# Kernel tuning notes

Measured on AMD Instinct MI355X. Metric: run time of the kernel, lower is better.

Reference implementation:

```python
import jax, jax.numpy as jnp
import numpy as np

DIM = 768
NUM_HEADS = 12
HEAD_DIM = DIM // NUM_HEADS
SCALE = HEAD_DIM ** -0.5
N, B = 1024, 8


def setup_inputs() -> dict:
    key = jax.random.key(0)
    ks = jax.random.split(key, 10)
    s = 0.02
    return {
        "q": jax.random.normal(ks[0], (N, B, DIM), jnp.float32),
        "k": jax.random.normal(ks[1], (N, B, DIM), jnp.float32),
        "v": jax.random.normal(ks[2], (N, B, DIM), jnp.float32),
        "v_img": jax.random.normal(ks[3], (N, B, DIM), jnp.float32),
        "Wq": jax.random.normal(ks[4], (DIM, DIM), jnp.float32) * s,
        "Wk": jax.random.normal(ks[5], (DIM, DIM), jnp.float32) * s,
        "Wv": jax.random.normal(ks[6], (DIM, DIM), jnp.float32) * s,
        "Wvim": jax.random.normal(ks[7], (DIM, DIM), jnp.float32) * s,
        "Wp": jax.random.normal(ks[8], (DIM, DIM), jnp.float32) * s,
        "bp": jnp.zeros((DIM,), jnp.float32),
        "Wpi": jax.random.normal(ks[9], (DIM, DIM), jnp.float32) * s,
        "bpi": jnp.zeros((DIM,), jnp.float32),
    }


def _heads(x):
    # [B, N, C] -> [B, H, N, Dh]
    b, n, _ = x.shape
    return x.reshape(b, n, NUM_HEADS, HEAD_DIM).transpose(0, 2, 1, 3)


def _merge(x):
    # [B, H, N, Dh] -> [B, N, C]
    b, h, n, d = x.shape
    return x.transpose(0, 2, 1, 3).reshape(b, n, h * d)


def reference(q, k, v, v_img, Wq, Wk, Wv, Wvim, Wp, bp, Wpi, bpi):
    # seq-first [N, B, C] -> batch-first [B, N, C]
    qb = jnp.transpose(q, (1, 0, 2)) @ Wq.T
    kb = jnp.transpose(k, (1, 0, 2)) @ Wk.T
    vb = jnp.transpose(v, (1, 0, 2)) @ Wv.T
    vib = jnp.transpose(v_img, (1, 0, 2)) @ Wvim.T

    qh, kh, vh, vih = _heads(qb), _heads(kb), _heads(vb), _heads(vib)

    # shared attention matrix, reused for both value streams
    attn = jnp.einsum("bhqd,bhkd->bhqk", qh, kh) * SCALE
    attn = jax.nn.softmax(attn, axis=-1)

    x = _merge(jnp.einsum("bhqk,bhkd->bhqd", attn, vh)) @ Wp.T + bp
    x_im = _merge(jnp.einsum("bhqk,bhkd->bhqd", attn, vih)) @ Wpi.T + bpi
    return (x, x_im)
```

## Files before the change

kernel.cpp:

```cpp
#include <hip/hip_runtime.h>

#define NSEQ 1024
#define BATCH 8
#define DIMC 768
#define NH 12
#define HD 64
#define SEG 6291456
#define WSEG 589824

typedef __attribute__((ext_vector_type(4))) float f32x4;
typedef __attribute__((ext_vector_type(8))) short s16x8;
typedef __attribute__((ext_vector_type(8))) __bf16 bf16x8;

#define GLL16(gsrc, ldst) __builtin_amdgcn_global_load_lds( \
    (const __attribute__((address_space(1))) unsigned int*)(const void*)(gsrc), \
    (__attribute__((address_space(3))) unsigned int*)(void*)(ldst), 16, 0, 0)

__device__ __forceinline__ short f2bf(float f) {
  union { float f; unsigned u; } v; v.f = f;
  unsigned r = (v.u + 0x7FFFu + ((v.u >> 16) & 1u)) >> 16;
  return (short)r;
}

__device__ __forceinline__ short f2bf1(float f) {
  unsigned r;
  asm("v_cvt_pk_bf16_f32 %0, %1, %2" : "=v"(r) : "v"(f), "v"(0.f));
  return (short)r;
}

__device__ __forceinline__ f32x4 mfma16(bf16x8 a, bf16x8 b, f32x4 c) {
  return __builtin_amdgcn_mfma_f32_16x16x32_bf16(a, b, c, 0, 0, 0);
}

__global__ __launch_bounds__(256) void k_cvt4(
    const float* __restrict__ a0, const float* __restrict__ a1,
    const float* __restrict__ a2, const float* __restrict__ a3,
    short* __restrict__ b0, short* __restrict__ b1,
    short* __restrict__ b2, short* __restrict__ b3, int n4) {
  const float* src; short* dst;
  switch (blockIdx.y) {
    case 0: src = a0; dst = b0; break;
    case 1: src = a1; dst = b1; break;
    case 2: src = a2; dst = b2; break;
    default: src = a3; dst = b3; break;
  }
  int i = blockIdx.x * 256 + threadIdx.x;
  if (i >= n4) return;
  float4 f = reinterpret_cast<const float4*>(src)[i];
  short4 o;
  o.x = f2bf(f.x); o.y = f2bf(f.y); o.z = f2bf(f.z); o.w = f2bf(f.w);
  reinterpret_cast<short4*>(dst)[i] = o;
}

__global__ __launch_bounds__(256) void k_proj(
    const short* __restrict__ x0, const short* __restrict__ x1,
    const short* __restrict__ x2, const short* __restrict__ x3,
    const short* __restrict__ w0, const short* __restrict__ w1,
    const short* __restrict__ w2, const short* __restrict__ w3,
    short* __restrict__ y0, short* __restrict__ y1,
    short* __restrict__ y2, short* __restrict__ y3) {
  __shared__ __align__(16) short SM[32768];
  const int tid = threadIdx.x;
  const int lane = tid & 63;
  const int w = tid >> 6;
  const int wm = w >> 1, wn = w & 1;
  const int nt = blockIdx.x, mt = blockIdx.y, s = blockIdx.z;
  const short *X, *W; short* Y;
  if (s == 0)      { X = x0; W = w0; Y = y0; }
  else if (s == 1) { X = x1; W = w1; Y = y1; }
  else if (s == 2) { X = x2; W = w2; Y = y2; }
  else             { X = x3; W = w3; Y = y3; }

  f32x4 acc[4][4];
#pragma unroll
  for (int mi = 0; mi < 4; ++mi)
#pragma unroll
    for (int ni = 0; ni < 4; ++ni) acc[mi][ni] = (f32x4){0.f, 0.f, 0.f, 0.f};

#define PROJ_STAGE(BUF, KT) do { \
  _Pragma("unroll") for (int ii = 0; ii < 4; ++ii) { \
    int g = ii * 256 + tid; \
    int o = g * 16; \
    int r = o >> 7; \
    int c0 = ((o & 127) ^ ((r & 7) << 4)) >> 1; \
    int m = mt * 128 + r; \
    GLL16(X + ((size_t)((m & 1023) * BATCH + (m >> 10))) * DIMC + (KT) * 64 + c0, \
          (char*)(SM + (BUF) * 8192) + o); \
    GLL16(W + (size_t)(nt * 128 + r) * DIMC + (KT) * 64 + c0, \
          (char*)(SM + 16384 + (BUF) * 8192) + o); \
  } \
} while (0)

  PROJ_STAGE(0, 0);
  __syncthreads();
  int buf = 0;
  for (int kt = 0; kt < 12; ++kt) {
    if (kt < 11) PROJ_STAGE(buf ^ 1, kt + 1);
    const char* As = (const char*)(SM + buf * 8192);
    const char* Bs = (const char*)(SM + 16384 + buf * 8192);
#pragma unroll
    for (int kk = 0; kk < 2; ++kk) {
      bf16x8 a[4], b[4];
      int ce = kk * 32 + (lane >> 4) * 8;
#pragma unroll
      for (int mi = 0; mi < 4; ++mi) {
        int ra = wm * 64 + mi * 16 + (lane & 15);
        int byte = ((ra << 7) + (ce << 1)) ^ ((ra & 7) << 4);
        a[mi] = *(const bf16x8*)(As + byte);
      }
#pragma unroll
      for (int ni = 0; ni < 4; ++ni) {
        int rb = wn * 64 + ni * 16 + (lane & 15);
        int byte = ((rb << 7) + (ce << 1)) ^ ((rb & 7) << 4);
        b[ni] = *(const bf16x8*)(Bs + byte);
      }
#pragma unroll
      for (int mi = 0; mi < 4; ++mi)
#pragma unroll
        for (int ni = 0; ni < 4; ++ni)
          acc[mi][ni] = mfma16(a[mi], b[ni], acc[mi][ni]);
    }
    __syncthreads();
    buf ^= 1;
  }
#undef PROJ_STAGE

  if (s < 2) {
#pragma unroll
    for (int mi = 0; mi < 4; ++mi)
#pragma unroll
      for (int ni = 0; ni < 4; ++ni)
#pragma unroll
        for (int j = 0; j < 4; ++j) {
          int m = mt * 128 + wm * 64 + mi * 16 + (lane >> 4) * 4 + j;
          int dc = nt * 128 + wn * 64 + ni * 16 + (lane & 15);
          int b_ = m >> 10, n_ = m & 1023;
          int h_ = dc >> 6, d_ = dc & 63;
          Y[((size_t)(b_ * NH + h_) * NSEQ + n_) * HD + d_] = f2bf(acc[mi][ni][j]);
        }
  } else {
    __syncthreads();
    short* Ts = SM;
#pragma unroll
    for (int mi = 0; mi < 4; ++mi)
#pragma unroll
      for (int ni = 0; ni < 4; ++ni)
#pragma unroll
        for (int j = 0; j < 4; ++j) {
          int lm = wm * 64 + mi * 16 + (lane >> 4) * 4 + j;
          int ldc = wn * 64 + ni * 16 + (lane & 15);
          int swc = ldc ^ (lm & 126);
          Ts[lm * 128 + swc] = f2bf(acc[mi][ni][j]);
        }
    __syncthreads();
    int l2 = lane * 2;
#pragma unroll 4
    for (int it = 0; it < 32; ++it) {
      int ldc = it * 4 + w;
      short2 pk;
      pk.x = Ts[l2 * 128 + (ldc ^ (l2 & 126))];
      pk.y = Ts[(l2 + 1) * 128 + (ldc ^ ((l2 + 1) & 126))];
      int dc = nt * 128 + ldc;
      int h_ = dc >> 6, d_ = dc & 63;
      int m = mt * 128 + l2;
      int b_ = m >> 10, n_ = m & 1023;
      *(short2*)(Y + ((size_t)(b_ * NH + h_) * HD + d_) * NSEQ + n_) = pk;
    }
  }
}

__global__ __launch_bounds__(256) void k_attn(
    const short* __restrict__ qh, const short* __restrict__ kh,
    const short* __restrict__ vt, const short* __restrict__ vit,
    short* __restrict__ xo, short* __restrict__ xio) {
  __shared__ __align__(16) short Ks[2][4096];
  __shared__ __align__(16) short Vs[2][4096];
  __shared__ __align__(16) short Vis[2][4096];
  __shared__ __align__(16) short Pl[4][2048];

  const int tid = threadIdx.x;
  const int lane = tid & 63;
  const int w = tid >> 6;
  const int blk = blockIdx.x;
  const int virt = (blk & 7) * 96 + (blk >> 3);
  const int bh = virt >> 3;
  const int qt = virt & 7;
  const float CF = 0.125f * 1.44269504f;

  const short* qbase = qh + ((size_t)bh * NSEQ + qt * 128 + w * 32) * HD;
  bf16x8 qf[2][2];
#pragma unroll
  for (int mi = 0; mi < 2; ++mi)
#pragma unroll
    for (int kq = 0; kq < 2; ++kq)
      qf[mi][kq] = *(const bf16x8*)(qbase + (mi * 16 + (lane & 15)) * HD + kq * 32 + (lane >> 4) * 8);

  bf16x8 onesf;
#pragma unroll
  for (int i = 0; i < 8; ++i) onesf[i] = (__bf16)1.0f;

  f32x4 o_[2][4], oi_[2][4], l_acc[2];
#pragma unroll
  for (int mi = 0; mi < 2; ++mi) {
    l_acc[mi] = (f32x4){0.f, 0.f, 0.f, 0.f};
#pragma unroll
    for (int x = 0; x < 4; ++x) {
      o_[mi][x] = (f32x4){0.f, 0.f, 0.f, 0.f};
      oi_[mi][x] = (f32x4){0.f, 0.f, 0.f, 0.f};
    }
  }

  const short* khb = kh + (size_t)bh * NSEQ * HD;
  const short* vtb = vt + (size_t)bh * NSEQ * HD;
  const short* vitb = vit + (size_t)bh * NSEQ * HD;
  char* PlW = (char*)&Pl[w][0];

#define ATTN_STAGE(BUF, KT) do { \
  _Pragma("unroll") for (int ii = 0; ii < 2; ++ii) { \
    int g = ii * 256 + tid; \
    int o = g * 16; \
    int r = o >> 7; \
    int c0 = ((o & 127) ^ ((r & 7) << 4)) >> 1; \
    GLL16(khb + (size_t)((KT) * 64 + r) * HD + c0, (char*)&Ks[BUF][0] + o); \
    GLL16(vtb + (size_t)r * NSEQ + (KT) * 64 + c0, (char*)&Vs[BUF][0] + o); \
    GLL16(vitb + (size_t)r * NSEQ + (KT) * 64 + c0, (char*)&Vis[BUF][0] + o); \
  } \
} while (0)

  ATTN_STAGE(0, 0);
  __syncthreads();
  int buf = 0;
  for (int kt = 0; kt < 16; ++kt) {
    if (kt < 15) ATTN_STAGE(buf ^ 1, kt + 1);
    const char* KsB = (const char*)&Ks[buf][0];
    const char* VsB = (const char*)&Vs[buf][0];
    const char* VisB = (const char*)&Vis[buf][0];

#pragma unroll
    for (int ni = 0; ni < 4; ++ni) {
      f32x4 s0 = (f32x4){0.f, 0.f, 0.f, 0.f};
      f32x4 s1 = (f32x4){0.f, 0.f, 0.f, 0.f};
#pragma unroll
      for (int kk = 0; kk < 2; ++kk) {
        int ce = kk * 32 + (lane >> 4) * 8;
        int rb = ni * 16 + (lane & 15);
        int byte = ((rb << 7) + (ce << 1)) ^ ((rb & 7) << 4);
        bf16x8 kfr = *(const bf16x8*)(KsB + byte);
        s0 = mfma16(qf[0][kk], kfr, s0);
        s1 = mfma16(qf[1][kk], kfr, s1);
      }
#pragma unroll
      for (int j = 0; j < 4; ++j) {
        float p0 = exp2f(s0[j] * CF);
        float p1 = exp2f(s1[j] * CF);
        int rw0 = (lane >> 4) * 4 + j;
        int col = ni * 16 + (lane & 15);
        int b0 = ((rw0 << 7) + (col << 1)) ^ ((rw0 & 7) << 4);
        int b1 = (((rw0 + 16) << 7) + (col << 1)) ^ ((rw0 & 7) << 4);
        *(short*)(PlW + b0) = f2bf1(p0);
        *(short*)(PlW + b1) = f2bf1(p1);
      }
    }

#pragma unroll
    for (int kk = 0; kk < 2; ++kk) {
      int co = kk * 32 + (lane >> 4) * 8;
      int r0 = lane & 15;
      int bp0 = ((r0 << 7) + (co << 1)) ^ ((r0 & 7) << 4);
      int bp1 = (((r0 + 16) << 7) + (co << 1)) ^ ((r0 & 7) << 4);
      bf16x8 pa0 = *(const bf16x8*)(PlW + bp0);
      bf16x8 pa1 = *(const bf16x8*)(PlW + bp1);
      l_acc[0] = mfma16(pa0, onesf, l_acc[0]);
      l_acc[1] = mfma16(pa1, onesf, l_acc[1]);
#pragma unroll
      for (int nd = 0; nd < 4; ++nd) {
        int rv = nd * 16 + (lane & 15);
        int byte = ((rv << 7) + (co << 1)) ^ ((rv & 7) << 4);
        bf16x8 vb = *(const bf16x8*)(VsB + byte);
        bf16x8 vib = *(const bf16x8*)(VisB + byte);
        o_[0][nd] = mfma16(pa0, vb, o_[0][nd]);
        o_[1][nd] = mfma16(pa1, vb, o_[1][nd]);
        oi_[0][nd] = mfma16(pa0, vib, oi_[0][nd]);
        oi_[1][nd] = mfma16(pa1, vib, oi_[1][nd]);
      }
    }
    __syncthreads();
    buf ^= 1;
  }
#undef ATTN_STAGE

#pragma unroll
  for (int mi = 0; mi < 2; ++mi)
#pragma unroll
    for (int j = 0; j < 4; ++j) {
      float inv = 1.0f / l_acc[mi][j];
      int n_ = qt * 128 + w * 32 + mi * 16 + (lane >> 4) * 4 + j;
      size_t base = ((size_t)bh * NSEQ + n_) * HD;
#pragma unroll
      for (int nd = 0; nd < 4; ++nd) {
        int d_ = nd * 16 + (lane & 15);
        xo[base + d_] = f2bf1(o_[mi][nd][j] * inv);
        xio[base + d_] = f2bf1(oi_[mi][nd][j] * inv);
      }
    }
}

__global__ __launch_bounds__(256) void k_outproj(
    const short* __restrict__ xa, const short* __restrict__ xb,
    const short* __restrict__ wa, const short* __restrict__ wb,
    const float* __restrict__ ba, const float* __restrict__ bb,
    float* __restrict__ out) {
  __shared__ __align__(16) short SM[32768];
  const int tid = threadIdx.x;
  const int lane = tid & 63;
  const int w = tid >> 6;
  const int wm = w >> 1, wn = w & 1;
  const int nt = blockIdx.x, mt = blockIdx.y, s = blockIdx.z;
  const short* X = (s == 0) ? xa : xb;
  const short* W = (s == 0) ? wa : wb;
  const float* bias = (s == 0) ? ba : bb;
  float* O = out + (size_t)s * SEG;

  f32x4 acc[4][4];
#pragma unroll
  for (int mi = 0; mi < 4; ++mi)
#pragma unroll
    for (int ni = 0; ni < 4; ++ni) acc[mi][ni] = (f32x4){0.f, 0.f, 0.f, 0.f};

#define OUTP_STAGE(BUF, KT) do { \
  _Pragma("unroll") for (int ii = 0; ii < 4; ++ii) { \
    int g = ii * 256 + tid; \
    int o = g * 16; \
    int r = o >> 7; \
    int c0 = ((o & 127) ^ ((r & 7) << 4)) >> 1; \
    int m = mt * 128 + r; \
    GLL16(X + (((size_t)(m >> 10) * NH + (KT)) * NSEQ + (m & 1023)) * HD + c0, \
          (char*)(SM + (BUF) * 8192) + o); \
    GLL16(W + (size_t)(nt * 128 + r) * DIMC + (KT) * 64 + c0, \
          (char*)(SM + 16384 + (BUF) * 8192) + o); \
  } \
} while (0)

  OUTP_STAGE(0, 0);
  __syncthreads();
  int buf = 0;
  for (int kt = 0; kt < 12; ++kt) {
    if (kt < 11) OUTP_STAGE(buf ^ 1, kt + 1);
    const char* As = (const char*)(SM + buf * 8192);
    const char* Bs = (const char*)(SM + 16384 + buf * 8192);
#pragma unroll
    for (int kk = 0; kk < 2; ++kk) {
      bf16x8 a[4], b[4];
      int ce = kk * 32 + (lane >> 4) * 8;
#pragma unroll
      for (int mi = 0; mi < 4; ++mi) {
        int ra = wm * 64 + mi * 16 + (lane & 15);
        int byte = ((ra << 7) + (ce << 1)) ^ ((ra & 7) << 4);
        a[mi] = *(const bf16x8*)(As + byte);
      }
#pragma unroll
      for (int ni = 0; ni < 4; ++ni) {
        int rb = wn * 64 + ni * 16 + (lane & 15);
        int byte = ((rb << 7) + (ce << 1)) ^ ((rb & 7) << 4);
        b[ni] = *(const bf16x8*)(Bs + byte);
      }
#pragma unroll
      for (int mi = 0; mi < 4; ++mi)
#pragma unroll
        for (int ni = 0; ni < 4; ++ni)
          acc[mi][ni] = mfma16(a[mi], b[ni], acc[mi][ni]);
    }
    __syncthreads();
    buf ^= 1;
  }
#undef OUTP_STAGE

#pragma unroll
  for (int mi = 0; mi < 4; ++mi)
#pragma unroll
    for (int ni = 0; ni < 4; ++ni)
#pragma unroll
      for (int j = 0; j < 4; ++j) {
        int m = mt * 128 + wm * 64 + mi * 16 + (lane >> 4) * 4 + j;
        int dc = nt * 128 + wn * 64 + ni * 16 + (lane & 15);
        O[(size_t)m * DIMC + dc] = acc[mi][ni][j] + bias[dc];
      }
}

extern "C" void kernel_launch(void* const* d_in, const int* in_sizes, int n_in,
                              void* d_out, int out_size, void* d_ws, size_t ws_size,
                              hipStream_t stream) {
  (void)in_sizes; (void)n_in; (void)out_size; (void)ws_size;
  const float* q    = (const float*)d_in[0];
  const float* k    = (const float*)d_in[1];
  const float* v    = (const float*)d_in[2];
  const float* vimg = (const float*)d_in[3];
  const float* Wq   = (const float*)d_in[4];
  const float* Wk   = (const float*)d_in[5];
  const float* Wv   = (const float*)d_in[6];
  const float* Wvim = (const float*)d_in[7];
  const float* Wp   = (const float*)d_in[8];
  const float* bp   = (const float*)d_in[9];
  const float* Wpi  = (const float*)d_in[10];
  const float* bpi  = (const float*)d_in[11];

  short* ws = (short*)d_ws;
  short* xq  = ws;
  short* xk  = ws + (size_t)SEG;
  short* xv  = ws + (size_t)2 * SEG;
  short* xvi = ws + (size_t)3 * SEG;
  short* wqb  = ws + (size_t)4 * SEG;
  short* wkb  = wqb + WSEG;
  short* wvb  = wkb + WSEG;
  short* wvib = wvb + WSEG;
  short* wpb  = wvib + WSEG;
  short* wpib = wpb + WSEG;
  short* qh  = ws + (size_t)4 * SEG + 6 * (size_t)WSEG;
  short* kh  = qh + (size_t)SEG;
  short* vht = kh + (size_t)SEG;
  short* viht = vht + (size_t)SEG;
  short* xo  = viht + (size_t)SEG;
  short* xio = xo + (size_t)SEG;

  k_cvt4<<<dim3(SEG / 4 / 256, 4), 256, 0, stream>>>(q, k, v, vimg, xq, xk, xv, xvi, SEG / 4);
  k_cvt4<<<dim3(WSEG / 4 / 256, 4), 256, 0, stream>>>(Wq, Wk, Wv, Wvim, wqb, wkb, wvb, wvib, WSEG / 4);
  k_cvt4<<<dim3(WSEG / 4 / 256, 2), 256, 0, stream>>>(Wp, Wpi, Wp, Wpi, wpb, wpib, wpb, wpib, WSEG / 4);

  k_proj<<<dim3(6, 64, 4), 256, 0, stream>>>(xq, xk, xv, xvi, wqb, wkb, wvb, wvib, qh, kh, vht, viht);

  k_attn<<<dim3(768), 256, 0, stream>>>(qh, kh, vht, viht, xo, xio);

  k_outproj<<<dim3(6, 64, 2), 256, 0, stream>>>(xo, xio, wpb, wpib, bp, bpi, (float*)d_out);
}
```

Before: 340.3 us.

## Keep softmax probabilities in registers via permlane swaps and fold scale into Wq

The attention kernel no longer writes exponentiated scores to LDS and reads them back. It swaps the QK^T MFMA operand order so results come out transposed, packs pairs to bf16 with v_cvt_pk_bf16_f32, and rearranges them with v_permlane32/16_swap to form PV operands directly in registers. The softmax scale times log2(e) is folded into the Wq bf16 conversion, which removes a multiply per score but changes where rounding happens. The projection grids are also reordered so blockIdx.x walks M tiles, which changes L2 reuse of weights versus activations.

```diff
diff --git a/kernel.cpp b/kernel.cpp
--- a/kernel.cpp
+++ b/kernel.cpp
@@ -9,6 +9,7 @@
 #define WSEG 589824
 
 typedef __attribute__((ext_vector_type(4))) float f32x4;
+typedef __attribute__((ext_vector_type(4))) unsigned u32x4;
 typedef __attribute__((ext_vector_type(8))) short s16x8;
 typedef __attribute__((ext_vector_type(8))) __bf16 bf16x8;
 
@@ -28,6 +29,12 @@
   return (short)r;
 }
 
+__device__ __forceinline__ unsigned cvtpk(float lo, float hi) {
+  unsigned r;
+  asm("v_cvt_pk_bf16_f32 %0, %1, %2" : "=v"(r) : "v"(lo), "v"(hi));
+  return r;
+}
+
 __device__ __forceinline__ f32x4 mfma16(bf16x8 a, bf16x8 b, f32x4 c) {
   return __builtin_amdgcn_mfma_f32_16x16x32_bf16(a, b, c, 0, 0, 0);
 }
@@ -36,19 +43,20 @@
     const float* __restrict__ a0, const float* __restrict__ a1,
     const float* __restrict__ a2, const float* __restrict__ a3,
     short* __restrict__ b0, short* __restrict__ b1,
-    short* __restrict__ b2, short* __restrict__ b3, int n4) {
-  const float* src; short* dst;
+    short* __restrict__ b2, short* __restrict__ b3, int n4,
+    float s0, float s1, float s2, float s3) {
+  const float* src; short* dst; float sc;
   switch (blockIdx.y) {
-    case 0: src = a0; dst = b0; break;
-    case 1: src = a1; dst = b1; break;
-    case 2: src = a2; dst = b2; break;
-    default: src = a3; dst = b3; break;
+    case 0: src = a0; dst = b0; sc = s0; break;
+    case 1: src = a1; dst = b1; sc = s1; break;
+    case 2: src = a2; dst = b2; sc = s2; break;
+    default: src = a3; dst = b3; sc = s3; break;
   }
   int i = blockIdx.x * 256 + threadIdx.x;
   if (i >= n4) return;
   float4 f = reinterpret_cast<const float4*>(src)[i];
   short4 o;
-  o.x = f2bf(f.x); o.y = f2bf(f.y); o.z = f2bf(f.z); o.w = f2bf(f.w);
+  o.x = f2bf(f.x * sc); o.y = f2bf(f.y * sc); o.z = f2bf(f.z * sc); o.w = f2bf(f.w * sc);
   reinterpret_cast<short4*>(dst)[i] = o;
 }
 
@@ -64,7 +72,7 @@
   const int lane = tid & 63;
   const int w = tid >> 6;
   const int wm = w >> 1, wn = w & 1;
-  const int nt = blockIdx.x, mt = blockIdx.y, s = blockIdx.z;
+  const int mt = blockIdx.x, nt = blockIdx.y, s = blockIdx.z;
   const short *X, *W; short* Y;
   if (s == 0)      { X = x0; W = w0; Y = y0; }
   else if (s == 1) { X = x1; W = w1; Y = y1; }
@@ -176,7 +184,6 @@
   __shared__ __align__(16) short Ks[2][4096];
   __shared__ __align__(16) short Vs[2][4096];
   __shared__ __align__(16) short Vis[2][4096];
-  __shared__ __align__(16) short Pl[4][2048];
 
   const int tid = threadIdx.x;
   const int lane = tid & 63;
@@ -185,7 +192,6 @@
   const int virt = (blk & 7) * 96 + (blk >> 3);
   const int bh = virt >> 3;
   const int qt = virt & 7;
-  const float CF = 0.125f * 1.44269504f;
 
   const short* qbase = qh + ((size_t)bh * NSEQ + qt * 128 + w * 32) * HD;
   bf16x8 qf[2][2];
@@ -213,7 +219,6 @@
   const short* khb = kh + (size_t)bh * NSEQ * HD;
   const short* vtb = vt + (size_t)bh * NSEQ * HD;
   const short* vitb = vit + (size_t)bh * NSEQ * HD;
-  char* PlW = (char*)&Pl[w][0];
 
 #define ATTN_STAGE(BUF, KT) do { \
   _Pragma("unroll") for (int ii = 0; ii < 2; ++ii) { \
@@ -236,6 +241,7 @@
     const char* VsB = (const char*)&Vs[buf][0];
     const char* VisB = (const char*)&Vis[buf][0];
 
+    unsigned pk0[2][4], pk1[2][4];
 #pragma unroll
     for (int ni = 0; ni < 4; ++ni) {
       f32x4 s0 = (f32x4){0.f, 0.f, 0.f, 0.f};
@@ -246,42 +252,45 @@
         int rb = ni * 16 + (lane & 15);
         int byte = ((rb << 7) + (ce << 1)) ^ ((rb & 7) << 4);
         bf16x8 kfr = *(const bf16x8*)(KsB + byte);
-        s0 = mfma16(qf[0][kk], kfr, s0);
-        s1 = mfma16(qf[1][kk], kfr, s1);
-      }
-#pragma unroll
-      for (int j = 0; j < 4; ++j) {
-        float p0 = exp2f(s0[j] * CF);
-        float p1 = exp2f(s1[j] * CF);
-        int rw0 = (lane >> 4) * 4 + j;
-        int col = ni * 16 + (lane & 15);
-        int b0 = ((rw0 << 7) + (col << 1)) ^ ((rw0 & 7) << 4);
-        int b1 = (((rw0 + 16) << 7) + (col << 1)) ^ ((rw0 & 7) << 4);
-        *(short*)(PlW + b0) = f2bf1(p0);
-        *(short*)(PlW + b1) = f2bf1(p1);
-      }
-    }
+        s0 = mfma16(kfr, qf[0][kk], s0);
+        s1 = mfma16(kfr, qf[1][kk], s1);
+      }
+      pk0[0][ni] = cvtpk(exp2f(s0[0]), exp2f(s0[1]));
+      pk1[0][ni] = cvtpk(exp2f(s0[2]), exp2f(s0[3]));
+      pk0[1][ni] = cvtpk(exp2f(s1[0]), exp2f(s1[1]));
+      pk1[1][ni] = cvtpk(exp2f(s1[2]), exp2f(s1[3]));
+    }
+
+    bf16x8 pa[2][2];
+#pragma unroll
+    for (int mi = 0; mi < 2; ++mi)
+#pragma unroll
+      for (int slot = 0; slot < 2; ++slot) {
+        unsigned a0 = pk0[mi][2 * slot], a1 = pk0[mi][2 * slot + 1];
+        asm("v_permlane32_swap_b32 %0, %1" : "+v"(a0), "+v"(a1));
+        asm("v_permlane16_swap_b32 %0, %1" : "+v"(a0), "+v"(a1));
+        unsigned b0 = pk1[mi][2 * slot], b1 = pk1[mi][2 * slot + 1];
+        asm("v_permlane32_swap_b32 %0, %1" : "+v"(b0), "+v"(b1));
+        asm("v_permlane16_swap_b32 %0, %1" : "+v"(b0), "+v"(b1));
+        u32x4 pw = (u32x4){a0, b0, a1, b1};
+        pa[mi][slot] = __builtin_bit_cast(bf16x8, pw);
+      }
 
 #pragma unroll
     for (int kk = 0; kk < 2; ++kk) {
       int co = kk * 32 + (lane >> 4) * 8;
-      int r0 = lane & 15;
-      int bp0 = ((r0 << 7) + (co << 1)) ^ ((r0 & 7) << 4);
-      int bp1 = (((r0 + 16) << 7) + (co << 1)) ^ ((r0 & 7) << 4);
-      bf16x8 pa0 = *(const bf16x8*)(PlW + bp0);
-      bf16x8 pa1 = *(const bf16x8*)(PlW + bp1);
-      l_acc[0] = mfma16(pa0, onesf, l_acc[0]);
-      l_acc[1] = mfma16(pa1, onesf, l_acc[1]);
+      l_acc[0] = mfma16(pa[0][kk], onesf, l_acc[0]);
+      l_acc[1] = mfma16(pa[1][kk], onesf, l_acc[1]);
 #pragma unroll
       for (int nd = 0; nd < 4; ++nd) {
         int rv = nd * 16 + (lane & 15);
         int byte = ((rv << 7) + (co << 1)) ^ ((rv & 7) << 4);
         bf16x8 vb = *(const bf16x8*)(VsB + byte);
         bf16x8 vib = *(const bf16x8*)(VisB + byte);
-        o_[0][nd] = mfma16(pa0, vb, o_[0][nd]);
-        o_[1][nd] = mfma16(pa1, vb, o_[1][nd]);
-        oi_[0][nd] = mfma16(pa0, vib, oi_[0][nd]);
-        oi_[1][nd] = mfma16(pa1, vib, oi_[1][nd]);
+        o_[0][nd] = mfma16(pa[0][kk], vb, o_[0][nd]);
+        o_[1][nd] = mfma16(pa[1][kk], vb, o_[1][nd]);
+        oi_[0][nd] = mfma16(pa[0][kk], vib, oi_[0][nd]);
+        oi_[1][nd] = mfma16(pa[1][kk], vib, oi_[1][nd]);
       }
     }
     __syncthreads();
@@ -315,7 +324,7 @@
   const int lane = tid & 63;
   const int w = tid >> 6;
   const int wm = w >> 1, wn = w & 1;
-  const int nt = blockIdx.x, mt = blockIdx.y, s = blockIdx.z;
+  const int mt = blockIdx.x, nt = blockIdx.y, s = blockIdx.z;
   const short* X = (s == 0) ? xa : xb;
   const short* W = (s == 0) ? wa : wb;
   const float* bias = (s == 0) ? ba : bb;
@@ -422,13 +431,18 @@
   short* xo  = viht + (size_t)SEG;
   short* xio = xo + (size_t)SEG;
 
-  k_cvt4<<<dim3(SEG / 4 / 256, 4), 256, 0, stream>>>(q, k, v, vimg, xq, xk, xv, xvi, SEG / 4);
-  k_cvt4<<<dim3(WSEG / 4 / 256, 4), 256, 0, stream>>>(Wq, Wk, Wv, Wvim, wqb, wkb, wvb, wvib, WSEG / 4);
-  k_cvt4<<<dim3(WSEG / 4 / 256, 2), 256, 0, stream>>>(Wp, Wpi, Wp, Wpi, wpb, wpib, wpb, wpib, WSEG / 4);
-
-  k_proj<<<dim3(6, 64, 4), 256, 0, stream>>>(xq, xk, xv, xvi, wqb, wkb, wvb, wvib, qh, kh, vht, viht);
+  const float SCL2E = 0.125f * 1.44269504f;
+
+  k_cvt4<<<dim3(SEG / 4 / 256, 4), 256, 0, stream>>>(q, k, v, vimg, xq, xk, xv, xvi, SEG / 4,
+                                                     1.f, 1.f, 1.f, 1.f);
+  k_cvt4<<<dim3(WSEG / 4 / 256, 4), 256, 0, stream>>>(Wq, Wk, Wv, Wvim, wqb, wkb, wvb, wvib, WSEG / 4,
+                                                      SCL2E, 1.f, 1.f, 1.f);
+  k_cvt4<<<dim3(WSEG / 4 / 256, 2), 256, 0, stream>>>(Wp, Wpi, Wp, Wpi, wpb, wpib, wpb, wpib, WSEG / 4,
+                                                      1.f, 1.f, 1.f, 1.f);
+
+  k_proj<<<dim3(64, 6, 4), 256, 0, stream>>>(xq, xk, xv, xvi, wqb, wkb, wvb, wvib, qh, kh, vht, viht);
 
   k_attn<<<dim3(768), 256, 0, stream>>>(qh, kh, vht, viht, xo, xio);
 
-  k_outproj<<<dim3(6, 64, 2), 256, 0, stream>>>(xo, xio, wpb, wpib, bp, bpi, (float*)d_out);
-}
+  k_outproj<<<dim3(64, 6, 2), 256, 0, stream>>>(xo, xio, wpb, wpib, bp, bpi, (float*)d_out);
+}
```

After: 314.1 us. 1.08x faster.
